# Performance work log

Measured on AMD Instinct MI355X. Metric: run time of the kernel, lower is better.

Reference implementation:

```python
import jax, jax.numpy as jnp
import numpy as np
import math

FACTOR = 5  # ProbAttention factor


def setup_inputs() -> dict:
    key = jax.random.key(0)
    kq, kk, kv = jax.random.split(key, 3)
    B, L, H, D = 4, 2048, 8, 64
    return {
        "queries": jax.random.normal(kq, (B, L, H, D), dtype=jnp.float32),
        "keys": jax.random.normal(kk, (B, L, H, D), dtype=jnp.float32),
        "values": jax.random.normal(kv, (B, L, H, D), dtype=jnp.float32),
    }


def reference(queries, keys, values):
    # queries/keys/values: [B, L, H, D] (self-attention, L == S)
    B, L, H, D = queries.shape
    S = keys.shape[1]
    Q = jnp.transpose(queries, (0, 2, 1, 3))  # [B,H,L,D]
    K = jnp.transpose(keys, (0, 2, 1, 3))     # [B,H,S,D]
    V = jnp.transpose(values, (0, 2, 1, 3))   # [B,H,S,D]

    # U: number of top queries kept; u: number of sampled keys per query
    n_top = min(max(1, int(FACTOR * math.log(max(S, 2)))), S, L)
    sample_k = min(max(1, int(FACTOR * math.log(max(L, 2)))), S)

    # --- _prob_QK: sampled QK, sparsity measure, top-k query selection ---
    idx_key = jax.random.key(42)  # matches torch.randint(L, (S, sample_k)) role
    index_sample = jax.random.randint(idx_key, (L, sample_k), 0, S)  # [L_Q, sample_k]
    K_sample = K[:, :, index_sample, :]                # [B,H,L,sample_k,D]
    QK_sample = jnp.einsum('bhqd,bhqjd->bhqj', Q, K_sample)  # [B,H,L,sample_k]
    # sparsity measure: max - mean (mean over full key length L_K = S)
    M = QK_sample.max(axis=-1) - QK_sample.sum(axis=-1) / S   # [B,H,L]
    M_top = jax.lax.top_k(M, n_top)[1]                 # [B,H,n_top] query indices
    Q_reduce = jnp.take_along_axis(Q, M_top[..., None], axis=2)  # [B,H,n_top,D]
    scores = jnp.einsum('bhud,bhkd->bhuk', Q_reduce, K)          # [B,H,n_top,S]

    scale = 1.0 / math.sqrt(D)
    scores = scores * scale

    # --- initial context: mask_flag=True and L_Q == L_V -> causal cumsum of V ---
    context = jnp.cumsum(V, axis=2)                    # [B,H,L,D]

    # --- masked softmax over selected queries (ProbMask: causal triu(1) rows) ---
    tri = jnp.triu(jnp.ones((S, S), dtype=bool), 1)    # [S,S]
    mask = tri[M_top]                                  # [B,H,n_top,S]
    scores = jnp.where(mask, -jnp.inf, scores)
    attn = jax.nn.softmax(scores, axis=-1)             # dropout is identity at eval
    attended = jnp.einsum('bhuk,bhkd->bhud', attn, V)  # [B,H,n_top,D]

    # --- scatter attended values into context at selected query positions ---
    b_idx = jnp.arange(B)[:, None, None]
    h_idx = jnp.arange(H)[None, :, None]
    context = context.at[b_idx, h_idx, M_top].set(attended)

    return jnp.transpose(context, (0, 2, 1, 3))        # [B,L,H,D]
```

## Files before the change

kernel.cpp:

```cpp
#include <hip/hip_runtime.h>
#include <hip/hip_bf16.h>
#include <math.h>

#define B_   4
#define L_   2048
#define H_   8
#define D_   64
#define NTOP 38
#define SAMPK 38


#define WS_M_OFF    0
#define WS_MTOP_OFF 262144
#define WS_SMALL    (WS_MTOP_OFF + 4864)
#define NSLOT8      (B_ * H_ * NTOP * 8)
#define WS8_PMAX    WS_SMALL
#define WS8_PSUM    (WS8_PMAX + NSLOT8 * 4)
#define WS8_PPV     (WS8_PSUM + NSLOT8 * 4)
#define WS8_TOTAL   (WS8_PPV + NSLOT8 * D_ * 4)
#define NSLOT16     (B_ * H_ * NTOP * 16)
#define WS16_PMAX   WS_SMALL
#define WS16_PSUM   (WS16_PMAX + NSLOT16 * 4)
#define WS16_PPV    (WS16_PSUM + NSLOT16 * 4)
#define WS16_TOTAL  (WS16_PPV + NSLOT16 * D_ * 4)

#define CHUNK16 128
#define SPITCH  132

__device__ __forceinline__ uint32_t rotl32(uint32_t v, int d) {
  return (v << d) | (v >> (32 - d));
}

__device__ __forceinline__ void threefry2x32(uint32_t k0, uint32_t k1,
                                             uint32_t x0, uint32_t x1,
                                             uint32_t& y0, uint32_t& y1) {
  const uint32_t ks2 = k0 ^ k1 ^ 0x1BD11BDAu;
  const uint32_t ks[3] = {k0, k1, ks2};
  x0 += k0; x1 += k1;
  const int ra[4] = {13, 15, 26, 6};
  const int rb[4] = {17, 29, 16, 24};
#pragma unroll
  for (int g = 0; g < 5; ++g) {
    const int* r = (g & 1) ? rb : ra;
#pragma unroll
    for (int i = 0; i < 4; ++i) {
      x0 += x1;
      x1 = rotl32(x1, r[i]);
      x1 ^= x0;
    }
    x0 += ks[(g + 1) % 3];
    x1 += ks[(g + 2) % 3] + (uint32_t)(g + 1);
  }
  y0 = x0; y1 = x1;
}

__device__ __forceinline__ int sample_idx(int t) {
  uint32_t k2_0, k2_1, y0, y1;
  threefry2x32(0u, 42u, 0u, 1u, k2_0, k2_1);
  threefry2x32(k2_0, k2_1, 0u, (uint32_t)t, y0, y1);
  return (int)((y0 ^ y1) & 2047u);
}

__global__ __launch_bounds__(256) void m_cumsum_kernel(const float* __restrict__ Q,
                                                       const float* __restrict__ K,
                                                       const float* __restrict__ V,
                                                       float* __restrict__ M,
                                                       float* __restrict__ out) {
  __shared__ uint16_t sidx[16][SAMPK];
  __shared__ float cs[8][32];

  int tid = threadIdx.x;

  if (blockIdx.x < 64) {
    int bI = blockIdx.x;
    int bh = bI >> 1, dhalf = bI & 1;
    int h = bh & (H_ - 1), b = bh >> 3;
    int dl = tid & 31, c = tid >> 5;
    const int CH = L_ / 8;
    int d = dhalf * 32 + dl;
    size_t base = ((size_t)b * L_ * H_ + h) * D_ + d;
    const size_t ls = (size_t)H_ * D_;
    float s = 0.f;
    for (int l = c * CH; l < (c + 1) * CH; ++l)
      s += V[base + (size_t)l * ls];
    cs[c][dl] = s;
    __syncthreads();
    float run = 0.f;
    for (int cc = 0; cc < c; ++cc) run += cs[cc][dl];
    for (int l = c * CH; l < (c + 1) * CH; ++l) {
      run += V[base + (size_t)l * ls];
      out[base + (size_t)l * ls] = run;
    }
    return;
  }

  int bI = blockIdx.x - 64;
  int j8 = bI >> 3;
  int bh = (bI & 7) + 8 * (j8 >> 7);
  int chunk = j8 & 127;
  int grp = tid >> 4, c = tid & 15;
  int q = chunk * 16 + grp;
  int h = bh & (H_ - 1), b = bh >> 3;

  for (int s = tid; s < 16 * SAMPK; s += 256) {
    int ql = s / SAMPK, jj = s - ql * SAMPK;
    sidx[ql][jj] = (uint16_t)sample_idx((chunk * 16 + ql) * SAMPK + jj);
  }
  __syncthreads();

  float4 qv = *(const float4*)(Q + (((size_t)b * L_ + q) * H_ + h) * D_ + 4 * c);
  const float* Kbase = K + ((size_t)b * L_ * H_ + h) * D_ + 4 * c;

  float mx = -1e30f, smv = 0.f;
  int j = 0;
  for (; j + 4 <= SAMPK; j += 4) {
    int r0 = (int)sidx[grp][j];
    int r1 = (int)sidx[grp][j + 1];
    int r2 = (int)sidx[grp][j + 2];
    int r3 = (int)sidx[grp][j + 3];
    float4 k0 = *(const float4*)(Kbase + (size_t)r0 * (H_ * D_));
    float4 k1 = *(const float4*)(Kbase + (size_t)r1 * (H_ * D_));
    float4 k2 = *(const float4*)(Kbase + (size_t)r2 * (H_ * D_));
    float4 k3 = *(const float4*)(Kbase + (size_t)r3 * (H_ * D_));
    float p0 = qv.x * k0.x + qv.y * k0.y + qv.z * k0.z + qv.w * k0.w;
    float p1 = qv.x * k1.x + qv.y * k1.y + qv.z * k1.z + qv.w * k1.w;
    float p2 = qv.x * k2.x + qv.y * k2.y + qv.z * k2.z + qv.w * k2.w;
    float p3 = qv.x * k3.x + qv.y * k3.y + qv.z * k3.z + qv.w * k3.w;
#pragma unroll
    for (int off = 1; off < 16; off <<= 1) {
      p0 += __shfl_xor(p0, off);
      p1 += __shfl_xor(p1, off);
      p2 += __shfl_xor(p2, off);
      p3 += __shfl_xor(p3, off);
    }
    mx = fmaxf(mx, p0); smv += p0;
    mx = fmaxf(mx, p1); smv += p1;
    mx = fmaxf(mx, p2); smv += p2;
    mx = fmaxf(mx, p3); smv += p3;
  }
  for (; j < SAMPK; ++j) {
    int r0 = (int)sidx[grp][j];
    float4 k0 = *(const float4*)(Kbase + (size_t)r0 * (H_ * D_));
    float p0 = qv.x * k0.x + qv.y * k0.y + qv.z * k0.z + qv.w * k0.w;
#pragma unroll
    for (int off = 1; off < 16; off <<= 1)
      p0 += __shfl_xor(p0, off);
    mx = fmaxf(mx, p0); smv += p0;
  }
  if (c == 0)
    M[(size_t)bh * L_ + q] = mx - smv * (1.0f / (float)L_);
}

__global__ __launch_bounds__(64) void topk_reg_kernel(const float* __restrict__ M,
                                                      int* __restrict__ mtop) {
  int bh = blockIdx.x;
  int lane = threadIdx.x;
  const float* Mrow = M + (size_t)bh * L_;

  float vals[32];
#pragma unroll
  for (int i = 0; i < 32; ++i)
    vals[i] = Mrow[lane + 64 * i];

  for (int u = 0; u < NTOP; ++u) {
    float bv = vals[0]; int bslot = 0;
#pragma unroll
    for (int i = 1; i < 32; ++i)
      if (vals[i] > bv) { bv = vals[i]; bslot = i; }
    float v = bv;
    int idx = lane + 64 * bslot;
#pragma unroll
    for (int off = 1; off < 64; off <<= 1) {
      float v2 = __shfl_xor(v, off);
      int   i2 = __shfl_xor(idx, off);
      if (v2 > v || (v2 == v && i2 < idx)) { v = v2; idx = i2; }
    }
    if (lane == 0) mtop[bh * NTOP + u] = idx;
    if ((idx & 63) == lane) {
      int slot = idx >> 6;
#pragma unroll
      for (int i = 0; i < 32; ++i)
        if (i == slot) vals[i] = -1e38f;
    }
  }
}

__global__ __launch_bounds__(512) void attn_split_kernel(const float* __restrict__ Q,
                                                         const float* __restrict__ K,
                                                         const float* __restrict__ V,
                                                         const int* __restrict__ mtop,
                                                         float* __restrict__ pmax,
                                                         float* __restrict__ psum,
                                                         float* __restrict__ ppv) {
  __shared__ float4 sK[CHUNK16 * 16];
  __shared__ float  sS[NTOP * SPITCH];
  __shared__ float4 sQ[NTOP * 16];
  __shared__ int    spos[NTOP];

  int bI = blockIdx.x;
  int c = bI & 15;
  int bh = bI >> 4;
  int h = bh & (H_ - 1), b = bh >> 3;
  int kstart = c * CHUNK16;
  int tid = threadIdx.x;

  int maxpos = -1;
  for (int u = 0; u < NTOP; ++u) {
    int p = mtop[bh * NTOP + u];
    maxpos = max(maxpos, p);
  }
  if (maxpos < kstart) return;

  const float* Kb = K + ((size_t)b * L_ * H_ + h) * D_;
  const float* Vb = V + ((size_t)b * L_ * H_ + h) * D_;
  const float* Qb = Q + ((size_t)b * L_ * H_ + h) * D_;

  if (tid < NTOP) {
    int p = mtop[bh * NTOP + tid];
    if (p < 0) p = 0;
    if (p > L_ - 1) p = L_ - 1;
    spos[tid] = p;
  }
  for (int s = tid; s < CHUNK16 * 16; s += 512) {
    int row = s >> 4, f = s & 15;
    sK[row * 16 + (f ^ (row & 15))] =
        *(const float4*)(Kb + (size_t)(kstart + row) * (H_ * D_) + 4 * f);
  }
  for (int s = tid; s < NTOP * 16; s += 512) {
    int u = s >> 4, f = s & 15;
    int p = mtop[bh * NTOP + u];
    if (p < 0) p = 0;
    if (p > L_ - 1) p = L_ - 1;
    sQ[s] = *(const float4*)(Qb + (size_t)p * (H_ * D_) + 4 * f);
  }
  __syncthreads();

  {
    int k = tid & 127;
    int ug = tid >> 7;
    float4 kreg[16];
#pragma unroll
    for (int f = 0; f < 16; ++f)
      kreg[f] = sK[k * 16 + (f ^ (k & 15))];

    int u0 = ug * 10, u1 = min(NTOP, u0 + 10);
    for (int u = u0; u < u1; ++u) {
      int pos = spos[u];
      if (pos < kstart) continue;
      int kloc = pos - kstart;
      float dot = 0.f;
#pragma unroll
      for (int f = 0; f < 16; ++f) {
        float4 qf = sQ[u * 16 + f];
        dot += kreg[f].x * qf.x + kreg[f].y * qf.y
             + kreg[f].z * qf.z + kreg[f].w * qf.w;
      }
      sS[u * SPITCH + k] = (k <= kloc) ? dot * 0.125f : -1e30f;
    }
  }
  __syncthreads();

  int w = tid >> 6, lane = tid & 63;
  int kq = lane >> 4, dq = lane & 15;
  for (int u = w; u < NTOP; u += 8) {
    int pos = spos[u];
    if (pos < kstart) continue;
    int kcnt = min(CHUNK16, pos + 1 - kstart);

    float s0 = sS[u * SPITCH + lane];
    float s1 = sS[u * SPITCH + 64 + lane];
    float m = fmaxf(s0, s1);
#pragma unroll
    for (int off = 1; off < 64; off <<= 1)
      m = fmaxf(m, __shfl_xor(m, off));
    float p0 = expf(s0 - m), p1 = expf(s1 - m);
    sS[u * SPITCH + lane] = p0;
    sS[u * SPITCH + 64 + lane] = p1;
    float sum = p0 + p1;
#pragma unroll
    for (int off = 1; off < 64; off <<= 1)
      sum += __shfl_xor(sum, off);

    float4 acc = make_float4(0.f, 0.f, 0.f, 0.f);
    for (int k0 = 0; k0 < kcnt; k0 += 4) {
      int kk = k0 + kq;
      if (kk < kcnt) {
        float p = sS[u * SPITCH + kk];
        float4 v4 = *(const float4*)(Vb + (size_t)(kstart + kk) * (H_ * D_) + 4 * dq);
        acc.x += p * v4.x; acc.y += p * v4.y;
        acc.z += p * v4.z; acc.w += p * v4.w;
      }
    }
    acc.x += __shfl_xor(acc.x, 16); acc.y += __shfl_xor(acc.y, 16);
    acc.z += __shfl_xor(acc.z, 16); acc.w += __shfl_xor(acc.w, 16);
    acc.x += __shfl_xor(acc.x, 32); acc.y += __shfl_xor(acc.y, 32);
    acc.z += __shfl_xor(acc.z, 32); acc.w += __shfl_xor(acc.w, 32);

    int slot = (bh * NTOP + u) * 16 + c;
    if (lane < 16)
      *(float4*)(ppv + (size_t)slot * D_ + 4 * lane) = acc;
    if (lane == 0) { pmax[slot] = m; psum[slot] = sum; }
  }
}

template <int NCHT>
__global__ __launch_bounds__(64) void attn_fin_kernel(const float* __restrict__ pmax,
                                                      const float* __restrict__ psum,
                                                      const float* __restrict__ ppv,
                                                      const int* __restrict__ mtop,
                                                      float* __restrict__ out) {
  const int CH = L_ / NCHT;
  int uu = blockIdx.x;
  int bh = uu / NTOP;
  int h = bh & (H_ - 1), b = bh >> 3;
  int pos = mtop[uu];
  if (pos < 0) pos = 0;
  if (pos > L_ - 1) pos = L_ - 1;
  int klen = pos + 1;
  int nch = (klen + CH - 1) / CH;
  int tid = threadIdx.x;

  int base = uu * NCHT;
  float gmax = -1e30f;
#pragma unroll
  for (int cc = 0; cc < NCHT; ++cc)
    if (cc < nch) gmax = fmaxf(gmax, pmax[base + cc]);

  float gsum = 0.f, acc = 0.f;
#pragma unroll
  for (int cc = 0; cc < NCHT; ++cc) {
    if (cc < nch) {
      float w0 = expf(pmax[base + cc] - gmax);
      gsum += psum[base + cc] * w0;
      acc += ppv[(size_t)(base + cc) * D_ + tid] * w0;
    }
  }
  out[(((size_t)b * L_ + pos) * H_ + h) * D_ + tid] = acc / gsum;
}

__global__ __launch_bounds__(256) void attn_part_kernel(const float* __restrict__ Q,
                                                        const float* __restrict__ K,
                                                        const float* __restrict__ V,
                                                        const int* __restrict__ mtop,
                                                        float* __restrict__ pmax,
                                                        float* __restrict__ psum,
                                                        float* __restrict__ ppv) {
  const int CHUNK = 256, NCH = 8;
  int bI = blockIdx.x;
  int c = bI & 7;
  int uu = bI >> 3;
  int bh = uu / NTOP;
  int h = bh & (H_ - 1), b = bh >> 3;

  int pos = mtop[uu];
  if (pos < 0) pos = 0;
  if (pos > L_ - 1) pos = L_ - 1;
  int klen = pos + 1;
  int kstart = c * CHUNK;
  if (kstart >= klen) return;
  int kcnt = min(CHUNK, klen - kstart);

  int tid = threadIdx.x;
  int c16 = tid & 15, g = tid >> 4;

  __shared__ float sc[CHUNK];
  __shared__ float red[256];
  __shared__ float4 part4[16][16];

  float4 qreg = *(const float4*)(Q + (((size_t)b * L_ + pos) * H_ + h) * D_ + 4 * c16);
  const float* Kbase = K + ((size_t)b * L_ * H_ + h) * D_ + 4 * c16;
  float lmax = -1e30f;
  for (int k = g; k < kcnt; k += 16) {
    float4 kv = *(const float4*)(Kbase + (size_t)(kstart + k) * (H_ * D_));
    float part = qreg.x * kv.x + qreg.y * kv.y + qreg.z * kv.z + qreg.w * kv.w;
#pragma unroll
    for (int off = 1; off < 16; off <<= 1)
      part += __shfl_xor(part, off);
    part *= 0.125f;
    if (c16 == 0) sc[k] = part;
    lmax = fmaxf(lmax, part);
  }
  red[tid] = lmax;
  __syncthreads();
  for (int s = 128; s > 0; s >>= 1) {
    if (tid < s) red[tid] = fmaxf(red[tid], red[tid + s]);
    __syncthreads();
  }
  float mx = red[0];
  __syncthreads();

  float lsum = 0.f;
  for (int k = tid; k < kcnt; k += 256) {
    float p = expf(sc[k] - mx);
    sc[k] = p;
    lsum += p;
  }
  red[tid] = lsum;
  __syncthreads();
  for (int s = 128; s > 0; s >>= 1) {
    if (tid < s) red[tid] += red[tid + s];
    __syncthreads();
  }
  float csum = red[0];
  __syncthreads();

  float4 acc = make_float4(0.f, 0.f, 0.f, 0.f);
  const float* Vbase = V + ((size_t)b * L_ * H_ + h) * D_ + 4 * c16;
  for (int k = g; k < kcnt; k += 16) {
    float p = sc[k];
    float4 v4 = *(const float4*)(Vbase + (size_t)(kstart + k) * (H_ * D_));
    acc.x += p * v4.x; acc.y += p * v4.y; acc.z += p * v4.z; acc.w += p * v4.w;
  }
  part4[g][c16] = acc;
  __syncthreads();
#pragma unroll
  for (int s = 8; s > 0; s >>= 1) {
    if (g < s) {
      float4 o = part4[g + s][c16];
      float4 m = part4[g][c16];
      m.x += o.x; m.y += o.y; m.z += o.z; m.w += o.w;
      part4[g][c16] = m;
    }
    __syncthreads();
  }

  int slot = uu * NCH + c;
  if (tid == 0) { pmax[slot] = mx; psum[slot] = csum; }
  if (tid < 16)
    *(float4*)(ppv + (size_t)slot * D_ + 4 * tid) = part4[0][tid];
}

__global__ __launch_bounds__(256) void m_kernel(const float* __restrict__ Q,
                                                const float* __restrict__ K,
                                                float* __restrict__ M) {
  int bI = blockIdx.x;
  int j8 = bI >> 3;
  int bh = (bI & 7) + 8 * (j8 >> 7);
  int chunk = j8 & 127;
  int tid = threadIdx.x;
  int grp = tid >> 4, c = tid & 15;
  int q = chunk * 16 + grp;
  int h = bh & (H_ - 1), b = bh >> 3;

  __shared__ uint16_t sidx[16][SAMPK];
  for (int s = tid; s < 16 * SAMPK; s += 256) {
    int ql = s / SAMPK, jj = s - ql * SAMPK;
    sidx[ql][jj] = (uint16_t)sample_idx((chunk * 16 + ql) * SAMPK + jj);
  }
  __syncthreads();

  float4 qv = *(const float4*)(Q + (((size_t)b * L_ + q) * H_ + h) * D_ + 4 * c);
  const float* Kbase = K + ((size_t)b * L_ * H_ + h) * D_ + 4 * c;

  float mx = -1e30f, smv = 0.f;
  for (int j = 0; j < SAMPK; ++j) {
    int row = (int)sidx[grp][j];
    float4 kv = *(const float4*)(Kbase + (size_t)row * (H_ * D_));
    float part = qv.x * kv.x + qv.y * kv.y + qv.z * kv.z + qv.w * kv.w;
#pragma unroll
    for (int off = 1; off < 16; off <<= 1)
      part += __shfl_xor(part, off);
    mx = fmaxf(mx, part);
    smv += part;
  }
  if (c == 0)
    M[(size_t)bh * L_ + q] = mx - smv * (1.0f / (float)L_);
}

__global__ __launch_bounds__(1024) void cumsum_kernel(const float* __restrict__ V,
                                                      float* __restrict__ out) {
  int bI = blockIdx.x;
  int bh = bI >> 1, dhalf = bI & 1;
  int h = bh & (H_ - 1), b = bh >> 3;
  int tid = threadIdx.x;
  int dl = tid & 31, c = tid >> 5;
  int d = dhalf * 32 + dl;
  const int CH = L_ / 32;
  __shared__ float cs[32][32];
  size_t base = ((size_t)b * L_ * H_ + h) * D_ + d;
  const size_t ls = (size_t)H_ * D_;
  float s = 0.f;
  for (int l = c * CH; l < (c + 1) * CH; ++l)
    s += V[base + (size_t)l * ls];
  cs[c][dl] = s;
  __syncthreads();
  float run = 0.f;
  for (int cc = 0; cc < c; ++cc) run += cs[cc][dl];
  for (int l = c * CH; l < (c + 1) * CH; ++l) {
    run += V[base + (size_t)l * ls];
    out[base + (size_t)l * ls] = run;
  }
}

__global__ __launch_bounds__(256) void topk_kernel(const float* __restrict__ M,
                                                   int* __restrict__ mtop) {
  int bh = blockIdx.x;
  int tid = threadIdx.x;
  __shared__ float sm[L_];
  __shared__ float wv[4];
  __shared__ int   wi[4];
  __shared__ int   ssel;
  const float* Mrow = M + (size_t)bh * L_;
  for (int i = tid; i < L_; i += 256) sm[i] = Mrow[i];
  __syncthreads();

  float bv = -1e38f; int bi = -1;
  for (int i = tid; i < L_; i += 256) {
    float v = sm[i];
    if (v > bv) { bv = v; bi = i; }
  }

  int lane = tid & 63, wid = tid >> 6;
  for (int u = 0; u < NTOP; ++u) {
    float v = bv; int i = bi;
#pragma unroll
    for (int off = 32; off > 0; off >>= 1) {
      float v2 = __shfl_down(v, off);
      int   i2 = __shfl_down(i, off);
      if (v2 > v || (v2 == v && i2 >= 0 && (i < 0 || i2 < i))) { v = v2; i = i2; }
    }
    if (lane == 0) { wv[wid] = v; wi[wid] = i; }
    __syncthreads();
    if (tid == 0) {
      float fv = wv[0]; int fi = wi[0];
#pragma unroll
      for (int w = 1; w < 4; ++w) {
        if (wv[w] > fv || (wv[w] == fv && wi[w] >= 0 && (fi < 0 || wi[w] < fi))) {
          fv = wv[w]; fi = wi[w];
        }
      }
      if (fi < 0) fi = 0;
      mtop[bh * NTOP + u] = fi;
      sm[fi] = -1e38f;
      ssel = fi;
    }
    __syncthreads();
    int sel = ssel;
    if (bi == sel) {
      bv = -1e38f; bi = -1;
      for (int i2 = tid; i2 < L_; i2 += 256) {
        float vv = sm[i2];
        if (vv > bv) { bv = vv; bi = i2; }
      }
    }
  }
}

__global__ __launch_bounds__(256) void attn_kernel(const float* __restrict__ Q,
                                                   const float* __restrict__ K,
                                                   const float* __restrict__ V,
                                                   const int* __restrict__ mtop,
                                                   float* __restrict__ out) {
  int bI = blockIdx.x;
  int j = bI >> 3;
  int u = j % NTOP;
  int bh = (bI & 7) + 8 * (j / NTOP);
  int h = bh & (H_ - 1), b = bh >> 3;
  int tid = threadIdx.x;

  int pos = mtop[bh * NTOP + u];
  if (pos < 0) pos = 0;
  if (pos > L_ - 1) pos = L_ - 1;
  int klen = pos + 1;

  __shared__ float qs[D_];
  __shared__ float sc[L_];
  __shared__ float redv[256];
  __shared__ float4 part4[16][16];

  if (tid < D_)
    qs[tid] = Q[(((size_t)b * L_ + pos) * H_ + h) * D_ + tid];
  __syncthreads();

  int c16 = tid & 15, g = tid >> 4;
  float4 qreg = *(const float4*)(qs + 4 * c16);
  const float* Kbase = K + ((size_t)b * L_ * H_ + h) * D_ + 4 * c16;
  float lmax = -1e30f;
  for (int k = g; k < klen; k += 16) {
    float4 kv = *(const float4*)(Kbase + (size_t)k * (H_ * D_));
    float part = qreg.x * kv.x + qreg.y * kv.y + qreg.z * kv.z + qreg.w * kv.w;
#pragma unroll
    for (int off = 1; off < 16; off <<= 1)
      part += __shfl_xor(part, off);
    part *= 0.125f;
    if (c16 == 0) sc[k] = part;
    lmax = fmaxf(lmax, part);
  }
  redv[tid] = lmax;
  __syncthreads();
  for (int s = 128; s > 0; s >>= 1) {
    if (tid < s) redv[tid] = fmaxf(redv[tid], redv[tid + s]);
    __syncthreads();
  }
  float mx = redv[0];
  __syncthreads();

  float lsum = 0.f;
  for (int k = tid; k < klen; k += 256) {
// ... 120 lines not shown
        float4 kv = k4[i];
        dot += qs[4 * i] * kv.x + qs[4 * i + 1] * kv.y
             + qs[4 * i + 2] * kv.z + qs[4 * i + 3] * kv.w;
      }
      dot *= 0.125f;
      sm[k] = dot;
      lmax = fmaxf(lmax, dot);
    }
    redv[tid] = lmax;
    __syncthreads();
    for (int s = 128; s > 0; s >>= 1) {
      if (tid < s) redv[tid] = fmaxf(redv[tid], redv[tid + s]);
      __syncthreads();
    }
    float mx = redv[0];
    __syncthreads();

    float lsum = 0.f;
    for (int k = tid; k < klen; k += 256) {
      float p = expf(sm[k] - mx);
      sm[k] = p;
      lsum += p;
    }
    redv[tid] = lsum;
    __syncthreads();
    for (int s = 128; s > 0; s >>= 1) {
      if (tid < s) redv[tid] += redv[tid + s];
      __syncthreads();
    }
    float inv = 1.0f / redv[0];
    __syncthreads();

    int d = tid & 63, slice = tid >> 6;
    float acc = 0.f;
    for (int k = slice; k < klen; k += 4)
      acc += sm[k] * V[(((size_t)b * L_ + k) * H_ + h) * D_ + d];
    part[slice][d] = acc;
    __syncthreads();
    if (tid < D_) {
      float r = (part[0][tid] + part[1][tid]) + (part[2][tid] + part[3][tid]);
      out[(((size_t)b * L_ + pos) * H_ + h) * D_ + tid] = r * inv;
    }
  }
}

extern "C" void kernel_launch(void* const* d_in, const int* in_sizes, int n_in,
                              void* d_out, int out_size, void* d_ws, size_t ws_size,
                              hipStream_t stream) {
  const float* Q = (const float*)d_in[0];
  const float* K = (const float*)d_in[1];
  const float* V = (const float*)d_in[2];
  float* out = (float*)d_out;

  if (ws_size >= (size_t)WS16_TOTAL) {
    char* ws = (char*)d_ws;
    float* M    = (float*)(ws + WS_M_OFF);
    int*   mt   = (int*)(ws + WS_MTOP_OFF);
    float* pmax = (float*)(ws + WS16_PMAX);
    float* psum = (float*)(ws + WS16_PSUM);
    float* ppv  = (float*)(ws + WS16_PPV);

    m_cumsum_kernel<<<4160, 256, 0, stream>>>(Q, K, V, M, out);
    topk_reg_kernel<<<B_ * H_, 64, 0, stream>>>(M, mt);
    attn_split_kernel<<<B_ * H_ * 16, 512, 0, stream>>>(Q, K, V, mt, pmax, psum, ppv);
    attn_fin_kernel<16><<<B_ * H_ * NTOP, 64, 0, stream>>>(pmax, psum, ppv, mt, out);
  } else if (ws_size >= (size_t)WS8_TOTAL) {
    char* ws = (char*)d_ws;
    float* M    = (float*)(ws + WS_M_OFF);
    int*   mt   = (int*)(ws + WS_MTOP_OFF);
    float* pmax = (float*)(ws + WS8_PMAX);
    float* psum = (float*)(ws + WS8_PSUM);
    float* ppv  = (float*)(ws + WS8_PPV);

    m_cumsum_kernel<<<4160, 256, 0, stream>>>(Q, K, V, M, out);
    topk_reg_kernel<<<B_ * H_, 64, 0, stream>>>(M, mt);
    attn_part_kernel<<<NSLOT8, 256, 0, stream>>>(Q, K, V, mt, pmax, psum, ppv);
    attn_fin_kernel<8><<<B_ * H_ * NTOP, 64, 0, stream>>>(pmax, psum, ppv, mt, out);
  } else if (ws_size >= (size_t)WS_SMALL) {
    char* ws = (char*)d_ws;
    float* M  = (float*)(ws + WS_M_OFF);
    int*   mt = (int*)(ws + WS_MTOP_OFF);

    m_kernel<<<4096, 256, 0, stream>>>(Q, K, M);
    topk_kernel<<<B_ * H_, 256, 0, stream>>>(M, mt);
    cumsum_kernel<<<B_ * H_ * 2, 1024, 0, stream>>>(V, out);
    attn_kernel<<<B_ * H_ * NTOP, 256, 0, stream>>>(Q, K, V, mt, out);
  } else {
    cumsum_kernel<<<B_ * H_ * 2, 1024, 0, stream>>>(V, out);
    fused_kernel<<<B_ * H_, 256, 0, stream>>>(Q, K, V, out);
  }
}
```

Measured before the change: 206.6 us.

## Fuse top-k into M kernel and merge split-attention finalize via last-block counters

Adds a new top path that runs the top-k selection inside the M/cumsum kernel, using an atomic per-(b,h) counter so the last finishing block computes top-k. The attention split kernel is rewritten with 64-key chunks (32 per head), handles all selected queries per block, and reduces the partial softmax results in its own last block, removing the separate topk and finalize launches. This trims launch overhead and inter-kernel gaps but adds a memset, atomics, thread fences and volatile reads. The path only runs if the workspace is large enough.

```diff
diff --git a/kernel.cpp b/kernel.cpp
--- a/kernel.cpp
+++ b/kernel.cpp
@@ -13,19 +13,24 @@
 #define WS_M_OFF    0
 #define WS_MTOP_OFF 262144
 #define WS_SMALL    (WS_MTOP_OFF + 4864)
-#define NSLOT8      (B_ * H_ * NTOP * 8)
-#define WS8_PMAX    WS_SMALL
-#define WS8_PSUM    (WS8_PMAX + NSLOT8 * 4)
-#define WS8_PPV     (WS8_PSUM + NSLOT8 * 4)
-#define WS8_TOTAL   (WS8_PPV + NSLOT8 * D_ * 4)
 #define NSLOT16     (B_ * H_ * NTOP * 16)
 #define WS16_PMAX   WS_SMALL
 #define WS16_PSUM   (WS16_PMAX + NSLOT16 * 4)
 #define WS16_PPV    (WS16_PSUM + NSLOT16 * 4)
 #define WS16_TOTAL  (WS16_PPV + NSLOT16 * D_ * 4)
+#define WS_CNT_OFF  267008
+#define WS32_BASE   267264
+#define NSLOT32     (B_ * H_ * NTOP * 32)
+#define WS32_PMAX   WS32_BASE
+#define WS32_PSUM   (WS32_PMAX + NSLOT32 * 4)
+#define WS32_PPV    (WS32_PSUM + NSLOT32 * 4)
+#define WS32_TOTAL  (WS32_PPV + NSLOT32 * D_ * 4)
 
 #define CHUNK16 128
 #define SPITCH  132
+#define CH32    64
+#define NCH32   32
+#define SP32    68
 
 __device__ __forceinline__ uint32_t rotl32(uint32_t v, int d) {
   return (v << d) | (v >> (32 - d));
@@ -61,13 +66,46 @@
   return (int)((y0 ^ y1) & 2047u);
 }
 
-__global__ __launch_bounds__(256) void m_cumsum_kernel(const float* __restrict__ Q,
-                                                       const float* __restrict__ K,
-                                                       const float* __restrict__ V,
-                                                       float* __restrict__ M,
-                                                       float* __restrict__ out) {
+__device__ __forceinline__ void topk38_wave(const volatile float* __restrict__ Mrow,
+                                            int lane, int* __restrict__ mrow_out) {
+  float vals[32];
+#pragma unroll
+  for (int i = 0; i < 32; ++i)
+    vals[i] = Mrow[lane + 64 * i];
+
+  for (int u = 0; u < NTOP; ++u) {
+    float bv = vals[0]; int bslot = 0;
+#pragma unroll
+    for (int i = 1; i < 32; ++i)
+      if (vals[i] > bv) { bv = vals[i]; bslot = i; }
+    float v = bv;
+    int idx = lane + 64 * bslot;
+#pragma unroll
+    for (int off = 1; off < 64; off <<= 1) {
+      float v2 = __shfl_xor(v, off);
+      int   i2 = __shfl_xor(idx, off);
+      if (v2 > v || (v2 == v && i2 < idx)) { v = v2; idx = i2; }
+    }
+    if (lane == 0) mrow_out[u] = idx;
+    if ((idx & 63) == lane) {
+      int slot = idx >> 6;
+#pragma unroll
+      for (int i = 0; i < 32; ++i)
+        if (i == slot) vals[i] = -1e38f;
+    }
+  }
+}
+
+__global__ __launch_bounds__(256) void m_cumsum_topk_kernel(const float* __restrict__ Q,
+                                                            const float* __restrict__ K,
+                                                            const float* __restrict__ V,
+                                                            float* __restrict__ M,
+                                                            float* __restrict__ out,
+                                                            int* __restrict__ mtop,
+                                                            int* __restrict__ cnt) {
   __shared__ uint16_t sidx[16][SAMPK];
   __shared__ float cs[8][32];
+  __shared__ int isLastS;
 
   int tid = threadIdx.x;
 
@@ -148,41 +186,252 @@
     mx = fmaxf(mx, p0); smv += p0;
   }
   if (c == 0)
+    atomicExch(&M[(size_t)bh * L_ + q], mx - smv * (1.0f / (float)L_));
+
+  __syncthreads();
+  if (tid == 0)
+    isLastS = (atomicAdd(&cnt[bh], 1) == 127);
+  __syncthreads();
+  if (!isLastS) return;
+  __threadfence();
+  if (tid < 64)
+    topk38_wave((const volatile float*)(M + (size_t)bh * L_), tid, mtop + bh * NTOP);
+}
+
+__global__ __launch_bounds__(512) void attn_split32_kernel(const float* __restrict__ Q,
+                                                           const float* __restrict__ K,
+                                                           const float* __restrict__ V,
+                                                           const int* __restrict__ mtop,
+                                                           float* __restrict__ pmax,
+                                                           float* __restrict__ psum,
+                                                           float* __restrict__ ppv,
+                                                           int* __restrict__ cnt,
+                                                           float* __restrict__ out) {
+  __shared__ float4 sK[CH32 * 16];
+  __shared__ float  sS[NTOP * SP32];
+  __shared__ float4 sQ[NTOP * 16];
+  __shared__ int    spos[NTOP];
+  __shared__ int    isLastS;
+
+  int bI = blockIdx.x;
+  int bh = (bI & 7) + 8 * (bI >> 8);
+  int c  = (bI >> 3) & 31;
+  int h = bh & (H_ - 1), b = bh >> 3;
+  int kstart = c * CH32;
+  int tid = threadIdx.x;
+
+  if (tid < NTOP) {
+    int p = mtop[bh * NTOP + tid];
+    if (p < 0) p = 0;
+    if (p > L_ - 1) p = L_ - 1;
+    spos[tid] = p;
+  }
+  __syncthreads();
+  int maxpos = 0;
+  for (int u = 0; u < NTOP; ++u) maxpos = max(maxpos, spos[u]);
+  bool active = (maxpos >= kstart);
+
+  if (active) {
+    const float* Kb = K + ((size_t)b * L_ * H_ + h) * D_;
+    const float* Qb = Q + ((size_t)b * L_ * H_ + h) * D_;
+    const float* Vb = V + ((size_t)b * L_ * H_ + h) * D_;
+
+    for (int s = tid; s < CH32 * 16; s += 512) {
+      int row = s >> 4, f = s & 15;
+      sK[row * 16 + (f ^ (row & 15))] =
+          *(const float4*)(Kb + (size_t)(kstart + row) * (H_ * D_) + 4 * f);
+    }
+    for (int s = tid; s < NTOP * 16; s += 512) {
+      int u = s >> 4, f = s & 15;
+      sQ[s] = *(const float4*)(Qb + (size_t)spos[u] * (H_ * D_) + 4 * f);
+    }
+    __syncthreads();
+
+    {
+      int k = tid & 63, ug = tid >> 6;
+      for (int u = ug; u < NTOP; u += 8) {
+        int pos = spos[u];
+        if (pos < kstart) continue;
+        int kloc = pos - kstart;
+        float dot = 0.f;
+#pragma unroll
+        for (int f = 0; f < 16; ++f) {
+          float4 kv = sK[k * 16 + (f ^ (k & 15))];
+          float4 qf = sQ[u * 16 + f];
+          dot += kv.x * qf.x + kv.y * qf.y + kv.z * qf.z + kv.w * qf.w;
+        }
+        sS[u * SP32 + k] = (k <= kloc) ? dot * 0.125f : -1e30f;
+      }
+    }
+    __syncthreads();
+
+    {
+      int w = tid >> 6, lane = tid & 63;
+      int kq = lane >> 4, dq = lane & 15;
+      for (int u = w; u < NTOP; u += 8) {
+        int pos = spos[u];
+        if (pos < kstart) continue;
+        int kcnt = min(CH32, pos + 1 - kstart);
+        float s0 = sS[u * SP32 + lane];
+        float m = s0;
+#pragma unroll
+        for (int off = 1; off < 64; off <<= 1)
+          m = fmaxf(m, __shfl_xor(m, off));
+        float p0 = expf(s0 - m);
+        sS[u * SP32 + lane] = p0;
+        float sum = p0;
+#pragma unroll
+        for (int off = 1; off < 64; off <<= 1)
+          sum += __shfl_xor(sum, off);
+
+        float4 acc = make_float4(0.f, 0.f, 0.f, 0.f);
+        for (int k0 = 0; k0 < kcnt; k0 += 4) {
+          int kk = k0 + kq;
+          if (kk < kcnt) {
+            float p = sS[u * SP32 + kk];
+            float4 v4 = *(const float4*)(Vb + (size_t)(kstart + kk) * (H_ * D_) + 4 * dq);
+            acc.x += p * v4.x; acc.y += p * v4.y;
+            acc.z += p * v4.z; acc.w += p * v4.w;
+          }
+        }
+        acc.x += __shfl_xor(acc.x, 16); acc.y += __shfl_xor(acc.y, 16);
+        acc.z += __shfl_xor(acc.z, 16); acc.w += __shfl_xor(acc.w, 16);
+        acc.x += __shfl_xor(acc.x, 32); acc.y += __shfl_xor(acc.y, 32);
+        acc.z += __shfl_xor(acc.z, 32); acc.w += __shfl_xor(acc.w, 32);
+
+        int slot = (bh * NTOP + u) * NCH32 + c;
+        if (lane < 16)
+          *(float4*)(ppv + (size_t)slot * D_ + 4 * lane) = acc;
+        if (lane == 0) { pmax[slot] = m; psum[slot] = sum; }
+      }
+    }
+  }
+
+  __syncthreads();
+  if (tid == 0) {
+    __threadfence();
+    isLastS = (atomicAdd(&cnt[bh], 1) == NCH32 - 1);
+  }
+  __syncthreads();
+  if (!isLastS) return;
+  __threadfence();
+
+  const volatile float* vpmax = pmax;
+  const volatile float* vpsum = psum;
+  const volatile float* vppv  = ppv;
+  int w = tid >> 6, lane = tid & 63;
+  for (int u = w; u < NTOP; u += 8) {
+    int pos = spos[u];
+    int nch = (pos + CH32) / CH32;
+    int base = (bh * NTOP + u) * NCH32;
+    float gmax = -1e30f;
+    for (int cc = 0; cc < nch; ++cc)
+      gmax = fmaxf(gmax, vpmax[base + cc]);
+    float gsum = 0.f, acc = 0.f;
+    for (int cc = 0; cc < nch; ++cc) {
+      float w0 = expf(vpmax[base + cc] - gmax);
+      gsum += vpsum[base + cc] * w0;
+      acc  += vppv[(size_t)(base + cc) * D_ + lane] * w0;
+    }
+    out[(((size_t)b * L_ + pos) * H_ + h) * D_ + lane] = acc / gsum;
+  }
+}
+
+__global__ __launch_bounds__(256) void m_cumsum_kernel(const float* __restrict__ Q,
+                                                       const float* __restrict__ K,
+                                                       const float* __restrict__ V,
+                                                       float* __restrict__ M,
+                                                       float* __restrict__ out) {
+  __shared__ uint16_t sidx[16][SAMPK];
+  __shared__ float cs[8][32];
+
+  int tid = threadIdx.x;
+
+  if (blockIdx.x < 64) {
+    int bI = blockIdx.x;
+    int bh = bI >> 1, dhalf = bI & 1;
+    int h = bh & (H_ - 1), b = bh >> 3;
+    int dl = tid & 31, c = tid >> 5;
+    const int CH = L_ / 8;
+    int d = dhalf * 32 + dl;
+    size_t base = ((size_t)b * L_ * H_ + h) * D_ + d;
+    const size_t ls = (size_t)H_ * D_;
+    float s = 0.f;
+    for (int l = c * CH; l < (c + 1) * CH; ++l)
+      s += V[base + (size_t)l * ls];
+    cs[c][dl] = s;
+    __syncthreads();
+    float run = 0.f;
+    for (int cc = 0; cc < c; ++cc) run += cs[cc][dl];
+    for (int l = c * CH; l < (c + 1) * CH; ++l) {
+      run += V[base + (size_t)l * ls];
+      out[base + (size_t)l * ls] = run;
+    }
+    return;
+  }
+
+  int bI = blockIdx.x - 64;
+  int j8 = bI >> 3;
+  int bh = (bI & 7) + 8 * (j8 >> 7);
+  int chunk = j8 & 127;
+  int grp = tid >> 4, c = tid & 15;
+  int q = chunk * 16 + grp;
+  int h = bh & (H_ - 1), b = bh >> 3;
+
+  for (int s = tid; s < 16 * SAMPK; s += 256) {
+    int ql = s / SAMPK, jj = s - ql * SAMPK;
+    sidx[ql][jj] = (uint16_t)sample_idx((chunk * 16 + ql) * SAMPK + jj);
+  }
+  __syncthreads();
+
+  float4 qv = *(const float4*)(Q + (((size_t)b * L_ + q) * H_ + h) * D_ + 4 * c);
+  const float* Kbase = K + ((size_t)b * L_ * H_ + h) * D_ + 4 * c;
+
+  float mx = -1e30f, smv = 0.f;
+  int j = 0;
+  for (; j + 4 <= SAMPK; j += 4) {
+    int r0 = (int)sidx[grp][j];
+    int r1 = (int)sidx[grp][j + 1];
+    int r2 = (int)sidx[grp][j + 2];
+    int r3 = (int)sidx[grp][j + 3];
+    float4 k0 = *(const float4*)(Kbase + (size_t)r0 * (H_ * D_));
+    float4 k1 = *(const float4*)(Kbase + (size_t)r1 * (H_ * D_));
+    float4 k2 = *(const float4*)(Kbase + (size_t)r2 * (H_ * D_));
+    float4 k3 = *(const float4*)(Kbase + (size_t)r3 * (H_ * D_));
+    float p0 = qv.x * k0.x + qv.y * k0.y + qv.z * k0.z + qv.w * k0.w;
+    float p1 = qv.x * k1.x + qv.y * k1.y + qv.z * k1.z + qv.w * k1.w;
+    float p2 = qv.x * k2.x + qv.y * k2.y + qv.z * k2.z + qv.w * k2.w;
+    float p3 = qv.x * k3.x + qv.y * k3.y + qv.z * k3.z + qv.w * k3.w;
+#pragma unroll
+    for (int off = 1; off < 16; off <<= 1) {
+      p0 += __shfl_xor(p0, off);
+      p1 += __shfl_xor(p1, off);
+      p2 += __shfl_xor(p2, off);
+      p3 += __shfl_xor(p3, off);
+    }
+    mx = fmaxf(mx, p0); smv += p0;
+    mx = fmaxf(mx, p1); smv += p1;
+    mx = fmaxf(mx, p2); smv += p2;
+    mx = fmaxf(mx, p3); smv += p3;
+  }
+  for (; j < SAMPK; ++j) {
+    int r0 = (int)sidx[grp][j];
+    float4 k0 = *(const float4*)(Kbase + (size_t)r0 * (H_ * D_));
+    float p0 = qv.x * k0.x + qv.y * k0.y + qv.z * k0.z + qv.w * k0.w;
+#pragma unroll
+    for (int off = 1; off < 16; off <<= 1)
+      p0 += __shfl_xor(p0, off);
+    mx = fmaxf(mx, p0); smv += p0;
+  }
+  if (c == 0)
     M[(size_t)bh * L_ + q] = mx - smv * (1.0f / (float)L_);
 }
 
 __global__ __launch_bounds__(64) void topk_reg_kernel(const float* __restrict__ M,
                                                       int* __restrict__ mtop) {
   int bh = blockIdx.x;
-  int lane = threadIdx.x;
-  const float* Mrow = M + (size_t)bh * L_;
-
-  float vals[32];
-#pragma unroll
-  for (int i = 0; i < 32; ++i)
-    vals[i] = Mrow[lane + 64 * i];
-
-  for (int u = 0; u < NTOP; ++u) {
-    float bv = vals[0]; int bslot = 0;
-#pragma unroll
-    for (int i = 1; i < 32; ++i)
-      if (vals[i] > bv) { bv = vals[i]; bslot = i; }
-    float v = bv;
-    int idx = lane + 64 * bslot;
-#pragma unroll
-    for (int off = 1; off < 64; off <<= 1) {
-      float v2 = __shfl_xor(v, off);
-      int   i2 = __shfl_xor(idx, off);
-      if (v2 > v || (v2 == v && i2 < idx)) { v = v2; idx = i2; }
-    }
-    if (lane == 0) mtop[bh * NTOP + u] = idx;
-    if ((idx & 63) == lane) {
-      int slot = idx >> 6;
-#pragma unroll
-      for (int i = 0; i < 32; ++i)
-        if (i == slot) vals[i] = -1e38f;
-    }
-  }
+  topk38_wave((const volatile float*)(M + (size_t)bh * L_), threadIdx.x,
+              mtop + bh * NTOP);
 }
 
 __global__ __launch_bounds__(512) void attn_split_kernel(const float* __restrict__ Q,
@@ -338,98 +587,6 @@
   out[(((size_t)b * L_ + pos) * H_ + h) * D_ + tid] = acc / gsum;
 }
 
-__global__ __launch_bounds__(256) void attn_part_kernel(const float* __restrict__ Q,
-                                                        const float* __restrict__ K,
-                                                        const float* __restrict__ V,
-                                                        const int* __restrict__ mtop,
-                                                        float* __restrict__ pmax,
-                                                        float* __restrict__ psum,
-                                                        float* __restrict__ ppv) {
-  const int CHUNK = 256, NCH = 8;
-  int bI = blockIdx.x;
-  int c = bI & 7;
-  int uu = bI >> 3;
-  int bh = uu / NTOP;
-  int h = bh & (H_ - 1), b = bh >> 3;
-
-  int pos = mtop[uu];
-  if (pos < 0) pos = 0;
-  if (pos > L_ - 1) pos = L_ - 1;
-  int klen = pos + 1;
-  int kstart = c * CHUNK;
-  if (kstart >= klen) return;
-  int kcnt = min(CHUNK, klen - kstart);
-
-  int tid = threadIdx.x;
-  int c16 = tid & 15, g = tid >> 4;
-
-  __shared__ float sc[CHUNK];
-  __shared__ float red[256];
-  __shared__ float4 part4[16][16];
-
-  float4 qreg = *(const float4*)(Q + (((size_t)b * L_ + pos) * H_ + h) * D_ + 4 * c16);
-  const float* Kbase = K + ((size_t)b * L_ * H_ + h) * D_ + 4 * c16;
-  float lmax = -1e30f;
-  for (int k = g; k < kcnt; k += 16) {
-    float4 kv = *(const float4*)(Kbase + (size_t)(kstart + k) * (H_ * D_));
-    float part = qreg.x * kv.x + qreg.y * kv.y + qreg.z * kv.z + qreg.w * kv.w;
-#pragma unroll
-    for (int off = 1; off < 16; off <<= 1)
-      part += __shfl_xor(part, off);
-    part *= 0.125f;
-    if (c16 == 0) sc[k] = part;
-    lmax = fmaxf(lmax, part);
-  }
-  red[tid] = lmax;
-  __syncthreads();
-  for (int s = 128; s > 0; s >>= 1) {
-    if (tid < s) red[tid] = fmaxf(red[tid], red[tid + s]);
-    __syncthreads();
-  }
-  float mx = red[0];
-  __syncthreads();
-
-  float lsum = 0.f;
-  for (int k = tid; k < kcnt; k += 256) {
-    float p = expf(sc[k] - mx);
-    sc[k] = p;
-    lsum += p;
-  }
-  red[tid] = lsum;
-  __syncthreads();
-  for (int s = 128; s > 0; s >>= 1) {
-    if (tid < s) red[tid] += red[tid + s];
-    __syncthreads();
-  }
-  float csum = red[0];
-  __syncthreads();
-
-  float4 acc = make_float4(0.f, 0.f, 0.f, 0.f);
-  const float* Vbase = V + ((size_t)b * L_ * H_ + h) * D_ + 4 * c16;
-  for (int k = g; k < kcnt; k += 16) {
-    float p = sc[k];
-    float4 v4 = *(const float4*)(Vbase + (size_t)(kstart + k) * (H_ * D_));
-    acc.x += p * v4.x; acc.y += p * v4.y; acc.z += p * v4.z; acc.w += p * v4.w;
-  }
-  part4[g][c16] = acc;
-  __syncthreads();
-#pragma unroll
-  for (int s = 8; s > 0; s >>= 1) {
-    if (g < s) {
-      float4 o = part4[g + s][c16];
-      float4 m = part4[g][c16];
-      m.x += o.x; m.y += o.y; m.z += o.z; m.w += o.w;
-      part4[g][c16] = m;
-    }
-    __syncthreads();
-  }
-
-  int slot = uu * NCH + c;
-  if (tid == 0) { pmax[slot] = mx; psum[slot] = csum; }
-  if (tid < 16)
-    *(float4*)(ppv + (size_t)slot * D_ + 4 * tid) = part4[0][tid];
-}
-
 __global__ __launch_bounds__(256) void m_kernel(const float* __restrict__ Q,
                                                 const float* __restrict__ K,
                                                 float* __restrict__ M) {
@@ -770,7 +927,20 @@
   const float* V = (const float*)d_in[2];
   float* out = (float*)d_out;
 
-  if (ws_size >= (size_t)WS16_TOTAL) {
+  if (ws_size >= (size_t)WS32_TOTAL) {
+    char* ws = (char*)d_ws;
+    float* M    = (float*)(ws + WS_M_OFF);
+    int*   mt   = (int*)(ws + WS_MTOP_OFF);
+    int*   cnt  = (int*)(ws + WS_CNT_OFF);
+    float* pmax = (float*)(ws + WS32_PMAX);
+    float* psum = (float*)(ws + WS32_PSUM);
+    float* ppv  = (float*)(ws + WS32_PPV);
+
+    hipMemsetAsync(cnt, 0, 256, stream);
+    m_cumsum_topk_kernel<<<4160, 256, 0, stream>>>(Q, K, V, M, out, mt, cnt);
+    attn_split32_kernel<<<1024, 512, 0, stream>>>(Q, K, V, mt, pmax, psum, ppv,
+                                                  cnt + 32, out);
+  } else if (ws_size >= (size_t)WS16_TOTAL) {
     char* ws = (char*)d_ws;
     float* M    = (float*)(ws + WS_M_OFF);
     int*   mt   = (int*)(ws + WS_MTOP_OFF);
@@ -782,18 +952,6 @@
     topk_reg_kernel<<<B_ * H_, 64, 0, stream>>>(M, mt);
     attn_split_kernel<<<B_ * H_ * 16, 512, 0, stream>>>(Q, K, V, mt, pmax, psum, ppv);
     attn_fin_kernel<16><<<B_ * H_ * NTOP, 64, 0, stream>>>(pmax, psum, ppv, mt, out);
-  } else if (ws_size >= (size_t)WS8_TOTAL) {
-    char* ws = (char*)d_ws;
-    float* M    = (float*)(ws + WS_M_OFF);
-    int*   mt   = (int*)(ws + WS_MTOP_OFF);
-    float* pmax = (float*)(ws + WS8_PMAX);
-    float* psum = (float*)(ws + WS8_PSUM);
-    float* ppv  = (float*)(ws + WS8_PPV);
-
-    m_cumsum_kernel<<<4160, 256, 0, stream>>>(Q, K, V, M, out);
-    topk_reg_kernel<<<B_ * H_, 64, 0, stream>>>(M, mt);
-    attn_part_kernel<<<NSLOT8, 256, 0, stream>>>(Q, K, V, mt, pmax, psum, ppv);
-    attn_fin_kernel<8><<<B_ * H_ * NTOP, 64, 0, stream>>>(pmax, psum, ppv, mt, out);
   } else if (ws_size >= (size_t)WS_SMALL) {
     char* ws = (char*)d_ws;
     float* M  = (float*)(ws + WS_M_OFF);
```

New measurement: 378.3 us. 83.1% more time.

## Fuse top-k selection into split attention kernel and hoist threefry key derivation

Applied to the files above, without the earlier changes.

Removes the separate top-k launch by having the first wave of every split-attention block compute the 38 top queries from M directly into LDS, while the other waves load the K chunk at the same time. Only chunk 0 writes the indices to global memory for the finalize kernel. The first threefry key derivation in the sampling loop is also hoisted out so it runs once per thread instead of once per sample. This saves one launch and a dependency gap, but the top-k work is now repeated in all 16 blocks per head and the early exit happens later, after the K tile has been loaded.

```diff
diff --git a/kernel.cpp b/kernel.cpp
--- a/kernel.cpp
+++ b/kernel.cpp
@@ -13,11 +13,6 @@
 #define WS_M_OFF    0
 #define WS_MTOP_OFF 262144
 #define WS_SMALL    (WS_MTOP_OFF + 4864)
-#define NSLOT8      (B_ * H_ * NTOP * 8)
-#define WS8_PMAX    WS_SMALL
-#define WS8_PSUM    (WS8_PMAX + NSLOT8 * 4)
-#define WS8_PPV     (WS8_PSUM + NSLOT8 * 4)
-#define WS8_TOTAL   (WS8_PPV + NSLOT8 * D_ * 4)
 #define NSLOT16     (B_ * H_ * NTOP * 16)
 #define WS16_PMAX   WS_SMALL
 #define WS16_PSUM   (WS16_PMAX + NSLOT16 * 4)
@@ -59,6 +54,76 @@
   threefry2x32(0u, 42u, 0u, 1u, k2_0, k2_1);
   threefry2x32(k2_0, k2_1, 0u, (uint32_t)t, y0, y1);
   return (int)((y0 ^ y1) & 2047u);
+}
+
+__device__ __forceinline__ int sample_idx_k2(uint32_t k2_0, uint32_t k2_1, int t) {
+  uint32_t y0, y1;
+  threefry2x32(k2_0, k2_1, 0u, (uint32_t)t, y0, y1);
+  return (int)((y0 ^ y1) & 2047u);
+}
+
+__device__ __forceinline__ void topk38_wave_lds(const float* __restrict__ Mrow,
+                                                int lane, int* __restrict__ spos,
+                                                int* __restrict__ mtop_g, bool writeG) {
+  float vals[32];
+#pragma unroll
+  for (int i = 0; i < 32; ++i)
+    vals[i] = Mrow[lane + 64 * i];
+
+  for (int u = 0; u < NTOP; ++u) {
+    float bv = vals[0]; int bslot = 0;
+#pragma unroll
+    for (int i = 1; i < 32; ++i)
+      if (vals[i] > bv) { bv = vals[i]; bslot = i; }
+    float v = bv;
+    int idx = lane + 64 * bslot;
+#pragma unroll
+    for (int off = 1; off < 64; off <<= 1) {
+      float v2 = __shfl_xor(v, off);
+      int   i2 = __shfl_xor(idx, off);
+      if (v2 > v || (v2 == v && i2 < idx)) { v = v2; idx = i2; }
+    }
+    if (lane == 0) {
+      spos[u] = idx;
+      if (writeG) mtop_g[u] = idx;
+    }
+    if ((idx & 63) == lane) {
+      int slot = idx >> 6;
+#pragma unroll
+      for (int i = 0; i < 32; ++i)
+        if (i == slot) vals[i] = -1e38f;
+    }
+  }
+}
+
+__device__ __forceinline__ void topk38_wave(const float* __restrict__ Mrow,
+                                            int lane, int* __restrict__ mrow_out) {
+  float vals[32];
+#pragma unroll
+  for (int i = 0; i < 32; ++i)
+    vals[i] = Mrow[lane + 64 * i];
+
+  for (int u = 0; u < NTOP; ++u) {
+    float bv = vals[0]; int bslot = 0;
+#pragma unroll
+    for (int i = 1; i < 32; ++i)
+      if (vals[i] > bv) { bv = vals[i]; bslot = i; }
+    float v = bv;
+    int idx = lane + 64 * bslot;
+#pragma unroll
+    for (int off = 1; off < 64; off <<= 1) {
+      float v2 = __shfl_xor(v, off);
+      int   i2 = __shfl_xor(idx, off);
+      if (v2 > v || (v2 == v && i2 < idx)) { v = v2; idx = i2; }
+    }
+    if (lane == 0) mrow_out[u] = idx;
+    if ((idx & 63) == lane) {
+      int slot = idx >> 6;
+#pragma unroll
+      for (int i = 0; i < 32; ++i)
+        if (i == slot) vals[i] = -1e38f;
+    }
+  }
 }
 
 __global__ __launch_bounds__(256) void m_cumsum_kernel(const float* __restrict__ Q,
@@ -102,9 +167,14 @@
   int q = chunk * 16 + grp;
   int h = bh & (H_ - 1), b = bh >> 3;
 
-  for (int s = tid; s < 16 * SAMPK; s += 256) {
-    int ql = s / SAMPK, jj = s - ql * SAMPK;
-    sidx[ql][jj] = (uint16_t)sample_idx((chunk * 16 + ql) * SAMPK + jj);
+  {
+    uint32_t k2_0, k2_1;
+    threefry2x32(0u, 42u, 0u, 1u, k2_0, k2_1);
+    for (int s = tid; s < 16 * SAMPK; s += 256) {
+      int ql = s / SAMPK, jj = s - ql * SAMPK;
+      sidx[ql][jj] =
+          (uint16_t)sample_idx_k2(k2_0, k2_1, (chunk * 16 + ql) * SAMPK + jj);
+    }
   }
   __syncthreads();
 
@@ -151,47 +221,14 @@
     M[(size_t)bh * L_ + q] = mx - smv * (1.0f / (float)L_);
 }
 
-__global__ __launch_bounds__(64) void topk_reg_kernel(const float* __restrict__ M,
-                                                      int* __restrict__ mtop) {
-  int bh = blockIdx.x;
-  int lane = threadIdx.x;
-  const float* Mrow = M + (size_t)bh * L_;
-
-  float vals[32];
-#pragma unroll
-  for (int i = 0; i < 32; ++i)
-    vals[i] = Mrow[lane + 64 * i];
-
-  for (int u = 0; u < NTOP; ++u) {
-    float bv = vals[0]; int bslot = 0;
-#pragma unroll
-    for (int i = 1; i < 32; ++i)
-      if (vals[i] > bv) { bv = vals[i]; bslot = i; }
-    float v = bv;
-    int idx = lane + 64 * bslot;
-#pragma unroll
-    for (int off = 1; off < 64; off <<= 1) {
-      float v2 = __shfl_xor(v, off);
-      int   i2 = __shfl_xor(idx, off);
-      if (v2 > v || (v2 == v && i2 < idx)) { v = v2; idx = i2; }
-    }
-    if (lane == 0) mtop[bh * NTOP + u] = idx;
-    if ((idx & 63) == lane) {
-      int slot = idx >> 6;
-#pragma unroll
-      for (int i = 0; i < 32; ++i)
-        if (i == slot) vals[i] = -1e38f;
-    }
-  }
-}
-
-__global__ __launch_bounds__(512) void attn_split_kernel(const float* __restrict__ Q,
-                                                         const float* __restrict__ K,
-                                                         const float* __restrict__ V,
-                                                         const int* __restrict__ mtop,
-                                                         float* __restrict__ pmax,
-                                                         float* __restrict__ psum,
-                                                         float* __restrict__ ppv) {
+__global__ __launch_bounds__(512) void attn_split_tk_kernel(const float* __restrict__ Q,
+                                                            const float* __restrict__ K,
+                                                            const float* __restrict__ V,
+                                                            const float* __restrict__ M,
+                                                            int* __restrict__ mtop,
+                                                            float* __restrict__ pmax,
+                                                            float* __restrict__ psum,
+                                                            float* __restrict__ ppv) {
   __shared__ float4 sK[CHUNK16 * 16];
   __shared__ float  sS[NTOP * SPITCH];
   __shared__ float4 sQ[NTOP * 16];
@@ -204,34 +241,28 @@
   int kstart = c * CHUNK16;
   int tid = threadIdx.x;
 
-  int maxpos = -1;
-  for (int u = 0; u < NTOP; ++u) {
-    int p = mtop[bh * NTOP + u];
-    maxpos = max(maxpos, p);
-  }
-  if (maxpos < kstart) return;
-
   const float* Kb = K + ((size_t)b * L_ * H_ + h) * D_;
   const float* Vb = V + ((size_t)b * L_ * H_ + h) * D_;
   const float* Qb = Q + ((size_t)b * L_ * H_ + h) * D_;
 
-  if (tid < NTOP) {
-    int p = mtop[bh * NTOP + tid];
-    if (p < 0) p = 0;
-    if (p > L_ - 1) p = L_ - 1;
-    spos[tid] = p;
-  }
-  for (int s = tid; s < CHUNK16 * 16; s += 512) {
-    int row = s >> 4, f = s & 15;
-    sK[row * 16 + (f ^ (row & 15))] =
-        *(const float4*)(Kb + (size_t)(kstart + row) * (H_ * D_) + 4 * f);
-  }
+  if (tid < 64) {
+    topk38_wave_lds(M + (size_t)bh * L_, tid, spos, mtop + bh * NTOP, c == 0);
+  } else {
+    for (int s = tid - 64; s < CHUNK16 * 16; s += 448) {
+      int row = s >> 4, f = s & 15;
+      sK[row * 16 + (f ^ (row & 15))] =
+          *(const float4*)(Kb + (size_t)(kstart + row) * (H_ * D_) + 4 * f);
+    }
+  }
+  __syncthreads();
+
+  int maxpos = 0;
+  for (int u = 0; u < NTOP; ++u) maxpos = max(maxpos, spos[u]);
+  if (maxpos < kstart) return;
+
   for (int s = tid; s < NTOP * 16; s += 512) {
     int u = s >> 4, f = s & 15;
-    int p = mtop[bh * NTOP + u];
-    if (p < 0) p = 0;
-    if (p > L_ - 1) p = L_ - 1;
-    sQ[s] = *(const float4*)(Qb + (size_t)p * (H_ * D_) + 4 * f);
+    sQ[s] = *(const float4*)(Qb + (size_t)spos[u] * (H_ * D_) + 4 * f);
   }
   __syncthreads();
 
@@ -338,98 +369,6 @@
   out[(((size_t)b * L_ + pos) * H_ + h) * D_ + tid] = acc / gsum;
 }
 
-__global__ __launch_bounds__(256) void attn_part_kernel(const float* __restrict__ Q,
-                                                        const float* __restrict__ K,
-                                                        const float* __restrict__ V,
-                                                        const int* __restrict__ mtop,
-                                                        float* __restrict__ pmax,
-                                                        float* __restrict__ psum,
-                                                        float* __restrict__ ppv) {
-  const int CHUNK = 256, NCH = 8;
-  int bI = blockIdx.x;
-  int c = bI & 7;
-  int uu = bI >> 3;
-  int bh = uu / NTOP;
-  int h = bh & (H_ - 1), b = bh >> 3;
-
-  int pos = mtop[uu];
-  if (pos < 0) pos = 0;
-  if (pos > L_ - 1) pos = L_ - 1;
-  int klen = pos + 1;
-  int kstart = c * CHUNK;
-  if (kstart >= klen) return;
-  int kcnt = min(CHUNK, klen - kstart);
-
-  int tid = threadIdx.x;
-  int c16 = tid & 15, g = tid >> 4;
-
-  __shared__ float sc[CHUNK];
-  __shared__ float red[256];
-  __shared__ float4 part4[16][16];
-
-  float4 qreg = *(const float4*)(Q + (((size_t)b * L_ + pos) * H_ + h) * D_ + 4 * c16);
-  const float* Kbase = K + ((size_t)b * L_ * H_ + h) * D_ + 4 * c16;
-  float lmax = -1e30f;
-  for (int k = g; k < kcnt; k += 16) {
-    float4 kv = *(const float4*)(Kbase + (size_t)(kstart + k) * (H_ * D_));
-    float part = qreg.x * kv.x + qreg.y * kv.y + qreg.z * kv.z + qreg.w * kv.w;
-#pragma unroll
-    for (int off = 1; off < 16; off <<= 1)
-      part += __shfl_xor(part, off);
-    part *= 0.125f;
-    if (c16 == 0) sc[k] = part;
-    lmax = fmaxf(lmax, part);
-  }
-  red[tid] = lmax;
-  __syncthreads();
-  for (int s = 128; s > 0; s >>= 1) {
-    if (tid < s) red[tid] = fmaxf(red[tid], red[tid + s]);
-    __syncthreads();
-  }
-  float mx = red[0];
-  __syncthreads();
-
-  float lsum = 0.f;
-  for (int k = tid; k < kcnt; k += 256) {
-    float p = expf(sc[k] - mx);
-    sc[k] = p;
-    lsum += p;
-  }
-  red[tid] = lsum;
-  __syncthreads();
-  for (int s = 128; s > 0; s >>= 1) {
-    if (tid < s) red[tid] += red[tid + s];
-    __syncthreads();
-  }
-  float csum = red[0];
-  __syncthreads();
-
-  float4 acc = make_float4(0.f, 0.f, 0.f, 0.f);
-  const float* Vbase = V + ((size_t)b * L_ * H_ + h) * D_ + 4 * c16;
-  for (int k = g; k < kcnt; k += 16) {
-    float p = sc[k];
-    float4 v4 = *(const float4*)(Vbase + (size_t)(kstart + k) * (H_ * D_));
-    acc.x += p * v4.x; acc.y += p * v4.y; acc.z += p * v4.z; acc.w += p * v4.w;
-  }
-  part4[g][c16] = acc;
-  __syncthreads();
-#pragma unroll
-  for (int s = 8; s > 0; s >>= 1) {
-    if (g < s) {
-      float4 o = part4[g + s][c16];
-      float4 m = part4[g][c16];
-      m.x += o.x; m.y += o.y; m.z += o.z; m.w += o.w;
-      part4[g][c16] = m;
-    }
-    __syncthreads();
-  }
-
-  int slot = uu * NCH + c;
-  if (tid == 0) { pmax[slot] = mx; psum[slot] = csum; }
-  if (tid < 16)
-    *(float4*)(ppv + (size_t)slot * D_ + 4 * tid) = part4[0][tid];
-}
-
 __global__ __launch_bounds__(256) void m_kernel(const float* __restrict__ Q,
                                                 const float* __restrict__ K,
                                                 float* __restrict__ M) {
@@ -492,58 +431,10 @@
   }
 }
 
-__global__ __launch_bounds__(256) void topk_kernel(const float* __restrict__ M,
-                                                   int* __restrict__ mtop) {
+__global__ __launch_bounds__(64) void topk_reg_kernel(const float* __restrict__ M,
+                                                      int* __restrict__ mtop) {
   int bh = blockIdx.x;
-  int tid = threadIdx.x;
-  __shared__ float sm[L_];
-  __shared__ float wv[4];
-  __shared__ int   wi[4];
-  __shared__ int   ssel;
-  const float* Mrow = M + (size_t)bh * L_;
-  for (int i = tid; i < L_; i += 256) sm[i] = Mrow[i];
-  __syncthreads();
-
-  float bv = -1e38f; int bi = -1;
-  for (int i = tid; i < L_; i += 256) {
-    float v = sm[i];
-    if (v > bv) { bv = v; bi = i; }
-  }
-
-  int lane = tid & 63, wid = tid >> 6;
-  for (int u = 0; u < NTOP; ++u) {
-    float v = bv; int i = bi;
-#pragma unroll
-    for (int off = 32; off > 0; off >>= 1) {
-      float v2 = __shfl_down(v, off);
-      int   i2 = __shfl_down(i, off);
-      if (v2 > v || (v2 == v && i2 >= 0 && (i < 0 || i2 < i))) { v = v2; i = i2; }
-    }
-    if (lane == 0) { wv[wid] = v; wi[wid] = i; }
-    __syncthreads();
-    if (tid == 0) {
-      float fv = wv[0]; int fi = wi[0];
-#pragma unroll
-      for (int w = 1; w < 4; ++w) {
-        if (wv[w] > fv || (wv[w] == fv && wi[w] >= 0 && (fi < 0 || wi[w] < fi))) {
-          fv = wv[w]; fi = wi[w];
-        }
-      }
-      if (fi < 0) fi = 0;
-      mtop[bh * NTOP + u] = fi;
-      sm[fi] = -1e38f;
-      ssel = fi;
-    }
-    __syncthreads();
-    int sel = ssel;
-    if (bi == sel) {
-      bv = -1e38f; bi = -1;
-      for (int i2 = tid; i2 < L_; i2 += 256) {
-        float vv = sm[i2];
-        if (vv > bv) { bv = vv; bi = i2; }
-      }
-    }
-  }
+  topk38_wave(M + (size_t)bh * L_, threadIdx.x, mtop + bh * NTOP);
 }
 
 __global__ __launch_bounds__(256) void attn_kernel(const float* __restrict__ Q,
@@ -779,28 +670,16 @@
     float* ppv  = (float*)(ws + WS16_PPV);
 
     m_cumsum_kernel<<<4160, 256, 0, stream>>>(Q, K, V, M, out);
-    topk_reg_kernel<<<B_ * H_, 64, 0, stream>>>(M, mt);
-    attn_split_kernel<<<B_ * H_ * 16, 512, 0, stream>>>(Q, K, V, mt, pmax, psum, ppv);
+    attn_split_tk_kernel<<<B_ * H_ * 16, 512, 0, stream>>>(Q, K, V, M, mt,
+                                                           pmax, psum, ppv);
     attn_fin_kernel<16><<<B_ * H_ * NTOP, 64, 0, stream>>>(pmax, psum, ppv, mt, out);
-  } else if (ws_size >= (size_t)WS8_TOTAL) {
-    char* ws = (char*)d_ws;
-    float* M    = (float*)(ws + WS_M_OFF);
-    int*   mt   = (int*)(ws + WS_MTOP_OFF);
-    float* pmax = (float*)(ws + WS8_PMAX);
-    float* psum = (float*)(ws + WS8_PSUM);
-    float* ppv  = (float*)(ws + WS8_PPV);
-
-    m_cumsum_kernel<<<4160, 256, 0, stream>>>(Q, K, V, M, out);
-    topk_reg_kernel<<<B_ * H_, 64, 0, stream>>>(M, mt);
-    attn_part_kernel<<<NSLOT8, 256, 0, stream>>>(Q, K, V, mt, pmax, psum, ppv);
-    attn_fin_kernel<8><<<B_ * H_ * NTOP, 64, 0, stream>>>(pmax, psum, ppv, mt, out);
   } else if (ws_size >= (size_t)WS_SMALL) {
     char* ws = (char*)d_ws;
     float* M  = (float*)(ws + WS_M_OFF);
     int*   mt = (int*)(ws + WS_MTOP_OFF);
 
     m_kernel<<<4096, 256, 0, stream>>>(Q, K, M);
-    topk_kernel<<<B_ * H_, 256, 0, stream>>>(M, mt);
+    topk_reg_kernel<<<B_ * H_, 64, 0, stream>>>(M, mt);
     cumsum_kernel<<<B_ * H_ * 2, 1024, 0, stream>>>(V, out);
     attn_kernel<<<B_ * H_ * NTOP, 256, 0, stream>>>(Q, K, V, mt, out);
   } else {
```

Result: faster. 202.3 us (-2.1%).
